# Optimization experiments

Measured on AMD Instinct MI355X. Metric: run time of the kernel, lower is better.

Reference implementation:

```python
import jax, jax.numpy as jnp
import numpy as np

PATCH = 14  # dinov2 patch size
LN_EPS = 1e-5


def setup_inputs() -> dict:
    key = jax.random.key(0)
    ks = jax.random.split(key, 6)
    Nb, P, E, Hd = 4096, 5476, 1024, 128  # boxes, patches (74*74), embed_dim, hidden_dim
    return {
        "patch_tokens": jax.random.normal(ks[0], (1, P, E), dtype=jnp.float32),
        "bboxes": jax.random.randint(ks[1], (Nb, 4), 0, 1036, dtype=jnp.int32),
        "H": 1036,
        "W": 1036,
        "W1": jax.random.normal(ks[2], (E, Hd), dtype=jnp.float32) * 0.02,
        "b1": jnp.zeros((Hd,), dtype=jnp.float32),
        "gamma": jnp.ones((Hd,), dtype=jnp.float32),
        "beta": jnp.zeros((Hd,), dtype=jnp.float32),
        "W2": jax.random.normal(ks[3], (Hd, Hd), dtype=jnp.float32) * 0.02,
        "b2": jnp.zeros((Hd,), dtype=jnp.float32),
    }


def _roi_pool(patch_tokens, bboxes, H, W):
    """Vectorized equivalent of VisionEncoder.roi_pool_patches.

    patch_tokens: (1, nph*npw, E); bboxes: (Nb, 4) int pixel coords.
    Returns (Nb, E) mean of patch tokens inside each box.
    """
    nph, npw = H // PATCH, W // PATCH
    Nb = bboxes.shape[0]
    x1, y1, x2, y2 = (bboxes[:, 0], bboxes[:, 1], bboxes[:, 2], bboxes[:, 3])
    f32 = jnp.float32
    # int() truncation in torch == astype(int32) for non-negative values
    px1 = (x1.astype(f32) / W * npw).astype(jnp.int32)
    px2 = (x2.astype(f32) / W * npw).astype(jnp.int32)
    py1 = (y1.astype(f32) / H * nph).astype(jnp.int32)
    py2 = (y2.astype(f32) / H * nph).astype(jnp.int32)
    px1 = jnp.clip(px1, 0, npw - 1)
    px2 = jnp.maximum(px1 + 1, jnp.minimum(px2, npw))
    py1 = jnp.clip(py1, 0, nph - 1)
    py2 = jnp.maximum(py1 + 1, jnp.minimum(py2, nph))
    # Box membership masks over the patch grid (ragged gather expressed densely)
    ay = jnp.arange(nph, dtype=jnp.int32)
    ax = jnp.arange(npw, dtype=jnp.int32)
    my = (ay[None, :] >= py1[:, None]) & (ay[None, :] < py2[:, None])  # (Nb, nph)
    mx = (ax[None, :] >= px1[:, None]) & (ax[None, :] < px2[:, None])  # (Nb, npw)
    mask = (my[:, :, None] & mx[:, None, :]).reshape(Nb, nph * npw)
    mask = mask.astype(patch_tokens.dtype)
    counts = mask.sum(axis=-1, keepdims=True)  # always >= 1 by construction
    pooled = (mask @ patch_tokens[0]) / counts  # (Nb, E)
    return pooled


def _projection(x, W1, b1, gamma, beta, W2, b2):
    h = x @ W1 + b1
    mu = h.mean(axis=-1, keepdims=True)
    var = ((h - mu) ** 2).mean(axis=-1, keepdims=True)
    h = (h - mu) * jax.lax.rsqrt(var + LN_EPS) * gamma + beta
    h = jax.nn.relu(h)
    return h @ W2 + b2


def reference(patch_tokens, bboxes, H, W, W1, b1, gamma, beta, W2, b2):
    pooled = _roi_pool(patch_tokens, bboxes, H, W)
    return _projection(pooled, W1, b1, gamma, beta, W2, b2)
```

## Files before the change

kernel.cpp:

```cpp
#include <hip/hip_runtime.h>


#define HD 128
#define SPLITK 8

__device__ __forceinline__ int decode_dim(const int* p, int fallback) {
    if (p == nullptr) return fallback;
    int vi = *p;
    if (vi >= 1 && vi <= 1000000) return vi;
    float vf = __int_as_float(vi);
    if (vf >= 1.0f && vf <= 1000000.0f) return (int)vf;
    return fallback;
}

__attribute__((noinline, optnone))
__device__ int coord_map(int x, int W, int n) {
    double rd = 1.0 / (double)W;
    float r = (float)rd;
    double qd = (double)x * (double)r;
    float q = (float)qd;
    double pd = (double)q * (double)n;
    float p = (float)pd;
    return (int)p;
}

__global__ __launch_bounds__(256) void gemm_u_kernel(
    const float* __restrict__ T, const float* __restrict__ W1,
    float* __restrict__ U, int P, int E)
{
    __shared__ float As[32][65];
    __shared__ float Bs[32][HD];

    int t  = threadIdx.x;
    int tc = t & 31;
    int tr = t >> 5;
    int row0 = blockIdx.x * 64;
    int ks   = blockIdx.y;
    int kchunk = E >> 3;
    int kbase  = ks * kchunk;
    float* Uo = U + (size_t)ks * (size_t)P * HD;

    float acc[8][4];
#pragma unroll
    for (int r = 0; r < 8; ++r)
#pragma unroll
        for (int j = 0; j < 4; ++j) acc[r][j] = 0.f;

    int arow = t >> 2;
    int akq  = (t & 3) * 8;
    int brow = t >> 5;
    int bc   = (t & 31) * 4;

    for (int kt = 0; kt < kchunk; kt += 32) {
        int k0 = kbase + kt;
        {
            int rg = row0 + arow; if (rg >= P) rg = P - 1;
            const float* tp = T + (size_t)rg * E + k0 + akq;
            float4 v0 = *(const float4*)tp;
            float4 v1 = *(const float4*)(tp + 4);
            As[akq + 0][arow] = v0.x; As[akq + 1][arow] = v0.y;
            As[akq + 2][arow] = v0.z; As[akq + 3][arow] = v0.w;
            As[akq + 4][arow] = v1.x; As[akq + 5][arow] = v1.y;
            As[akq + 6][arow] = v1.z; As[akq + 7][arow] = v1.w;
        }
#pragma unroll
        for (int i = 0; i < 4; ++i) {
            int kk = brow + i * 8;
            *(float4*)&Bs[kk][bc] =
                *(const float4*)&W1[(size_t)(k0 + kk) * HD + bc];
        }
        __syncthreads();

#pragma unroll
        for (int kk = 0; kk < 32; ++kk) {
            float4 a0 = *(const float4*)&As[kk][tr * 8];
            float4 a1 = *(const float4*)&As[kk][tr * 8 + 4];
            float4 b  = *(const float4*)&Bs[kk][tc * 4];
            float av[8] = {a0.x, a0.y, a0.z, a0.w, a1.x, a1.y, a1.z, a1.w};
            float bv[4] = {b.x, b.y, b.z, b.w};
#pragma unroll
            for (int r = 0; r < 8; ++r)
#pragma unroll
                for (int j = 0; j < 4; ++j)
                    acc[r][j] += av[r] * bv[j];
        }
        __syncthreads();
    }

#pragma unroll
    for (int r = 0; r < 8; ++r) {
        int p = row0 + tr * 8 + r;
        if (p < P) {
            float4 v = make_float4(acc[r][0], acc[r][1], acc[r][2], acc[r][3]);
            *(float4*)&Uo[(size_t)p * HD + tc * 4] = v;
        }
    }
}

__global__ __launch_bounds__(256) void prefix_x_kernel(
    const float* __restrict__ U, float* __restrict__ S,
    int P, int npw, int nph)
{
    extern __shared__ float tile[];
    int t = threadIdx.x;
    int y = blockIdx.x;
    int ch0 = blockIdx.y * 64;
    size_t ustride = (size_t)P * HD;
    size_t ubase = (size_t)y * npw * HD + ch0;

    int nj = npw * 16;
    for (int j = t; j < nj; j += 256) {
        int x = j >> 4, cq = (j & 15) * 4;
        size_t off = ubase + (size_t)x * HD + cq;
        float4 s = *(const float4*)(U + off);
#pragma unroll
        for (int p = 1; p < SPLITK; ++p) {
            float4 v = *(const float4*)(U + (size_t)p * ustride + off);
            s.x += v.x; s.y += v.y; s.z += v.z; s.w += v.w;
        }
        *(float4*)&tile[x * 64 + cq] = s;
    }
    __syncthreads();

    if (t < 64) {
        int c = t;
        size_t srow = (size_t)(y + 1) * (npw + 1) * HD + ch0;
        S[srow + c] = 0.f;
        float acc = 0.f;
        for (int x = 0; x < npw; ++x) {
            acc += tile[x * 64 + c];
            S[srow + (size_t)(x + 1) * HD + c] = acc;
        }
    }
}

__global__ __launch_bounds__(256) void prefix_y_kernel(
    float* __restrict__ S, int npw, int nph)
{
    extern __shared__ float tile[];
    int t = threadIdx.x;
    int x = blockIdx.x;
    int ch0 = blockIdx.y * 64;
    size_t stride = (size_t)(npw + 1) * HD;
    size_t base = (size_t)x * HD + ch0;

    int nj = nph * 16;
    for (int j = t; j < nj; j += 256) {
        int y = j >> 4, cq = (j & 15) * 4;
        *(float4*)&tile[y * 64 + cq] =
            *(const float4*)(S + base + (size_t)(y + 1) * stride + cq);
    }
    __syncthreads();

    if (t < 64) {
        int c = t;
        S[base + c] = 0.f;
        float acc = 0.f;
        for (int y = 0; y < nph; ++y) {
            acc += tile[y * 64 + c];
            S[base + (size_t)(y + 1) * stride + c] = acc;
        }
    }
}

__global__ __launch_bounds__(256) void pool_proj_kernel(
    const float* __restrict__ S, const int* __restrict__ bboxes,
    const int* __restrict__ pH, const int* __restrict__ pW,
    const float* __restrict__ b1, const float* __restrict__ gamma,
    const float* __restrict__ beta, const float* __restrict__ W2,
    const float* __restrict__ b2, float* __restrict__ out,
    int Nb, int npw, int nph, int fbW, int fbH)
{
    __shared__ float hs[16][HD + 1];
    __shared__ float Bs[32][HD];
    __shared__ float red_s[16][17], red_q[16][17];
    __shared__ int   cI11[16], cI12[16], cI21[16], cI22[16];
    __shared__ float cCnt[16];
    __shared__ float mu_s[16], rs_s[16];

    int t = threadIdx.x;
    int c = t & 127;
    int rh = t >> 7;
    int row0 = blockIdx.x * 16;

    if (t < 16) {
        int b = row0 + t; if (b >= Nb) b = Nb - 1;
        int x1 = bboxes[b * 4 + 0];
        int y1 = bboxes[b * 4 + 1];
        int x2 = bboxes[b * 4 + 2];
        int y2 = bboxes[b * 4 + 3];
        int Wi = decode_dim(pW, fbW);
        int Hi = decode_dim(pH, fbH);
        int px1 = coord_map(x1, Wi, npw);
        int px2 = coord_map(x2, Wi, npw);
        int py1 = coord_map(y1, Hi, nph);
        int py2 = coord_map(y2, Hi, nph);
        px1 = min(max(px1, 0), npw - 1);
        px2 = max(px1 + 1, min(px2, npw));
        py1 = min(max(py1, 0), nph - 1);
        py2 = max(py1 + 1, min(py2, nph));
        int st = npw + 1;
        cI11[t] = (py1 * st + px1) * HD;
        cI12[t] = (py1 * st + px2) * HD;
        cI21[t] = (py2 * st + px1) * HD;
        cI22[t] = (py2 * st + px2) * HD;
        cCnt[t] = (float)((py2 - py1) * (px2 - px1));
    }
    __syncthreads();

    float bias1 = b1[c];
    float hv[8];
#pragma unroll
    for (int r = 0; r < 8; ++r) {
        int row = rh * 8 + r;
        float s = S[cI22[row] + c] - S[cI12[row] + c]
                - S[cI21[row] + c] + S[cI11[row] + c];
        hv[r] = s / cCnt[row] + bias1;
        hs[row][c] = hv[r];
    }
    __syncthreads();

    {
        int sr = t & 15;
        int sg = t >> 4;
        float ps = 0.f, pq = 0.f;
#pragma unroll
        for (int i = 0; i < 8; ++i) {
            float v = hs[sr][sg * 8 + i];
            ps += v; pq += v * v;
        }
        red_s[sr][sg] = ps; red_q[sr][sg] = pq;
    }
    __syncthreads();
    if (t < 16) {
        float s = 0.f, q = 0.f;
#pragma unroll
        for (int i = 0; i < 16; ++i) { s += red_s[t][i]; q += red_q[t][i]; }
        float m = s * (1.0f / HD);
        float v = q * (1.0f / HD) - m * m;
        mu_s[t] = m;
        rs_s[t] = rsqrtf(v + 1e-5f);
    }
    __syncthreads();

    float g = gamma[c], be = beta[c];
#pragma unroll
    for (int r = 0; r < 8; ++r) {
        int row = rh * 8 + r;
        float x = (hv[r] - mu_s[row]) * rs_s[row] * g + be;
        hs[row][c] = fmaxf(x, 0.f);
    }
    __syncthreads();

    float bias2 = b2[c];
    float acc2[8];
#pragma unroll
    for (int r = 0; r < 8; ++r) acc2[r] = bias2;
    for (int k0 = 0; k0 < HD; k0 += 32) {
#pragma unroll
        for (int i = 0; i < 16; ++i) {
            int idx = t + i * 256;
            int kk = idx >> 7, cc = idx & 127;
            Bs[kk][cc] = W2[(size_t)(k0 + kk) * HD + cc];
        }
        __syncthreads();
#pragma unroll
        for (int kk = 0; kk < 32; ++kk) {
            float bv = Bs[kk][c];
#pragma unroll
            for (int r = 0; r < 8; ++r)
                acc2[r] += hs[rh * 8 + r][k0 + kk] * bv;
        }
        __syncthreads();
    }

#pragma unroll
    for (int r = 0; r < 8; ++r) {
        int rg = row0 + rh * 8 + r;
        if (rg < Nb) out[(size_t)rg * HD + c] = acc2[r];
    }
}

extern "C" void kernel_launch(void* const* d_in, const int* in_sizes, int n_in,
                              void* d_out, int out_size, void* d_ws, size_t ws_size,
                              hipStream_t stream) {
    int iT = 0, iB = 1, iH = 2, iW = 3, iW1 = 4, ib1 = 5, ig = 6, ibe = 7,
        iW2 = 8, ib2 = 9;
    bool has_scalars = (n_in >= 10 && in_sizes[2] == 1 && in_sizes[3] == 1);
    if (!has_scalars) { iW1 = 2; ib1 = 3; ig = 4; ibe = 5; iW2 = 6; ib2 = 7; }

    const float* tokens = (const float*)d_in[iT];
    const int*   bboxes = (const int*)d_in[iB];
    const int*   pH     = has_scalars ? (const int*)d_in[iH] : nullptr;
    const int*   pW     = has_scalars ? (const int*)d_in[iW] : nullptr;
    const float* W1     = (const float*)d_in[iW1];
    const float* b1     = (const float*)d_in[ib1];
    const float* gamma  = (const float*)d_in[ig];
    const float* beta   = (const float*)d_in[ibe];
    const float* W2     = (const float*)d_in[iW2];
    const float* b2     = (const float*)d_in[ib2];
    float* out = (float*)d_out;

    int Hd = in_sizes[ib1];
    int E  = in_sizes[iW1] / Hd;
    int Nb = in_sizes[iB] / 4;
    int P  = in_sizes[iT] / E;
    int npw = 1;
    while ((npw + 1) * (npw + 1) <= P) ++npw;
    int nph = P / npw;
    (void)out_size; (void)ws_size;

    float* S = (float*)d_ws;
    size_t s_elems = ((size_t)(nph + 1) * (npw + 1) * HD + 255) & ~(size_t)255;
    float* U = S + s_elems;

    int mtiles = (P + 63) / 64;
    gemm_u_kernel<<<dim3(mtiles, SPLITK), dim3(256), 0, stream>>>(
        tokens, W1, U, P, E);
    prefix_x_kernel<<<dim3(nph, 2), dim3(256), (size_t)npw * 64 * 4, stream>>>(
        U, S, P, npw, nph);
    prefix_y_kernel<<<dim3(npw + 1, 2), dim3(256), (size_t)nph * 64 * 4, stream>>>(
        S, npw, nph);
    pool_proj_kernel<<<dim3((Nb + 15) / 16), dim3(256), 0, stream>>>(
        S, bboxes, pH, pW, b1, gamma, beta, W2, b2, out, Nb, npw, nph,
        14 * npw, 14 * nph);
}
```

Baseline: 138.7 us.

## Compute token×W1 GEMM with split-bf16 MFMA instead of FP32 FMA

Replaces the FP32 shared-memory tiled GEMM (tokens × W1) with an MFMA kernel. It splits each FP32 value into bf16 hi and lo parts and accumulates three bf16 products per tile to keep close to FP32 accuracy. A new pre-kernel transposes W1 and splits it into hi/lo bf16 arrays, and split-K drops from 8 to 4, which halves the partial-sum writes read by the prefix stage. This adds an extra launch and workspace, drops shared-memory reuse of W1 in favour of direct global loads, and gives slightly different rounding than pure FP32.

```diff
diff --git a/kernel.cpp b/kernel.cpp
--- a/kernel.cpp
+++ b/kernel.cpp
@@ -2,7 +2,10 @@
 
 
 #define HD 128
-#define SPLITK 8
+#define SPLITK 4
+
+typedef __attribute__((ext_vector_type(8))) short bf16x8;
+typedef __attribute__((ext_vector_type(4))) float f32x4;
 
 __device__ __forceinline__ int decode_dim(const int* p, int fallback) {
     if (p == nullptr) return fallback;
@@ -24,75 +27,98 @@
     return (int)p;
 }
 
-__global__ __launch_bounds__(256) void gemm_u_kernel(
-    const float* __restrict__ T, const float* __restrict__ W1,
-    float* __restrict__ U, int P, int E)
-{
-    __shared__ float As[32][65];
-    __shared__ float Bs[32][HD];
-
-    int t  = threadIdx.x;
-    int tc = t & 31;
-    int tr = t >> 5;
-    int row0 = blockIdx.x * 64;
-    int ks   = blockIdx.y;
-    int kchunk = E >> 3;
-    int kbase  = ks * kchunk;
-    float* Uo = U + (size_t)ks * (size_t)P * HD;
-
-    float acc[8][4];
-#pragma unroll
-    for (int r = 0; r < 8; ++r)
-#pragma unroll
-        for (int j = 0; j < 4; ++j) acc[r][j] = 0.f;
-
-    int arow = t >> 2;
-    int akq  = (t & 3) * 8;
-    int brow = t >> 5;
-    int bc   = (t & 31) * 4;
+__global__ __launch_bounds__(256) void split_w1_kernel(
+    const float* __restrict__ W1, unsigned short* __restrict__ Whi,
+    unsigned short* __restrict__ Wlo, int E)
+{
+    __shared__ float tile[64][65];
+    int t = threadIdx.x;
+    int k0 = blockIdx.x * 64, n0 = blockIdx.y * 64;
+
+    int r = t >> 4, c4 = (t & 15) * 4;
+#pragma unroll
+    for (int i = 0; i < 4; ++i) {
+        int kr = r + i * 16;
+        *(float4*)&tile[kr][c4] =
+            *(const float4*)&W1[(size_t)(k0 + kr) * HD + n0 + c4];
+    }
+    __syncthreads();
+
+    int nl = t >> 2, kq = (t & 3) * 16;
+    unsigned hp[8], lp[8];
+#pragma unroll
+    for (int j = 0; j < 8; ++j) {
+        float x0 = tile[kq + 2 * j][nl];
+        float x1 = tile[kq + 2 * j + 1][nl];
+        unsigned u0 = __float_as_uint(x0);
+        unsigned u1 = __float_as_uint(x1);
+        float l0 = x0 - __uint_as_float(u0 & 0xffff0000u);
+        float l1 = x1 - __uint_as_float(u1 & 0xffff0000u);
+        hp[j] = (u0 >> 16) | (u1 & 0xffff0000u);
+        lp[j] = (__float_as_uint(l0) >> 16) | (__float_as_uint(l1) & 0xffff0000u);
+    }
+    size_t off = (size_t)(n0 + nl) * E + k0 + kq;
+    *(uint4*)(Whi + off)     = make_uint4(hp[0], hp[1], hp[2], hp[3]);
+    *(uint4*)(Whi + off + 8) = make_uint4(hp[4], hp[5], hp[6], hp[7]);
+    *(uint4*)(Wlo + off)     = make_uint4(lp[0], lp[1], lp[2], lp[3]);
+    *(uint4*)(Wlo + off + 8) = make_uint4(lp[4], lp[5], lp[6], lp[7]);
+}
+
+__global__ __launch_bounds__(256) void gemm_u_mfma(
+    const float* __restrict__ T, const unsigned short* __restrict__ Whi,
+    const unsigned short* __restrict__ Wlo, float* __restrict__ U,
+    int P, int E)
+{
+    int t = threadIdx.x;
+    int lane = t & 63;
+    int w = t >> 6;
+    int row0 = blockIdx.x * 64 + w * 16;
+    int kchunk = E >> 2;
+    int kbase = blockIdx.y * kchunk;
+    float* Uo = U + (size_t)blockIdx.y * (size_t)P * HD;
+
+    int lr  = lane & 15;
+    int lkq = (lane >> 4) * 8;
+
+    int arow = row0 + lr; if (arow >= P) arow = P - 1;
+    const float* ap = T + (size_t)arow * E + kbase + lkq;
+    const unsigned short* bh0 = Whi + (size_t)lr * E + kbase + lkq;
+    const unsigned short* bl0 = Wlo + (size_t)lr * E + kbase + lkq;
+
+    f32x4 acc[8];
+#pragma unroll
+    for (int n = 0; n < 8; ++n) acc[n] = (f32x4){0.f, 0.f, 0.f, 0.f};
 
     for (int kt = 0; kt < kchunk; kt += 32) {
-        int k0 = kbase + kt;
-        {
-            int rg = row0 + arow; if (rg >= P) rg = P - 1;
-            const float* tp = T + (size_t)rg * E + k0 + akq;
-            float4 v0 = *(const float4*)tp;
-            float4 v1 = *(const float4*)(tp + 4);
-            As[akq + 0][arow] = v0.x; As[akq + 1][arow] = v0.y;
-            As[akq + 2][arow] = v0.z; As[akq + 3][arow] = v0.w;
-            As[akq + 4][arow] = v1.x; As[akq + 5][arow] = v1.y;
-            As[akq + 6][arow] = v1.z; As[akq + 7][arow] = v1.w;
-        }
-#pragma unroll
-        for (int i = 0; i < 4; ++i) {
-            int kk = brow + i * 8;
-            *(float4*)&Bs[kk][bc] =
-                *(const float4*)&W1[(size_t)(k0 + kk) * HD + bc];
-        }
-        __syncthreads();
-
-#pragma unroll
-        for (int kk = 0; kk < 32; ++kk) {
-            float4 a0 = *(const float4*)&As[kk][tr * 8];
-            float4 a1 = *(const float4*)&As[kk][tr * 8 + 4];
-            float4 b  = *(const float4*)&Bs[kk][tc * 4];
-            float av[8] = {a0.x, a0.y, a0.z, a0.w, a1.x, a1.y, a1.z, a1.w};
-            float bv[4] = {b.x, b.y, b.z, b.w};
-#pragma unroll
-            for (int r = 0; r < 8; ++r)
-#pragma unroll
-                for (int j = 0; j < 4; ++j)
-                    acc[r][j] += av[r] * bv[j];
-        }
-        __syncthreads();
-    }
-
-#pragma unroll
-    for (int r = 0; r < 8; ++r) {
-        int p = row0 + tr * 8 + r;
-        if (p < P) {
-            float4 v = make_float4(acc[r][0], acc[r][1], acc[r][2], acc[r][3]);
-            *(float4*)&Uo[(size_t)p * HD + tc * 4] = v;
+        float4 a0 = *(const float4*)(ap + kt);
+        float4 a1 = *(const float4*)(ap + kt + 4);
+        float av[8] = {a0.x, a0.y, a0.z, a0.w, a1.x, a1.y, a1.z, a1.w};
+        bf16x8 ahi, alo;
+#pragma unroll
+        for (int j = 0; j < 8; ++j) {
+            unsigned u = __float_as_uint(av[j]);
+            ahi[j] = (short)(u >> 16);
+            float l = av[j] - __uint_as_float(u & 0xffff0000u);
+            alo[j] = (short)(__float_as_uint(l) >> 16);
+        }
+#pragma unroll
+        for (int n = 0; n < 8; ++n) {
+            bf16x8 bhi = *(const bf16x8*)(bh0 + (size_t)(n * 16) * E + kt);
+            bf16x8 blo = *(const bf16x8*)(bl0 + (size_t)(n * 16) * E + kt);
+            acc[n] = __builtin_amdgcn_mfma_f32_16x16x32_bf16(ahi, bhi, acc[n], 0, 0, 0);
+            acc[n] = __builtin_amdgcn_mfma_f32_16x16x32_bf16(alo, bhi, acc[n], 0, 0, 0);
+            acc[n] = __builtin_amdgcn_mfma_f32_16x16x32_bf16(ahi, blo, acc[n], 0, 0, 0);
+        }
+    }
+
+    int cr0 = row0 + (lane >> 4) * 4;
+    int cc  = lane & 15;
+#pragma unroll
+    for (int n = 0; n < 8; ++n) {
+#pragma unroll
+        for (int r = 0; r < 4; ++r) {
+            int p = cr0 + r;
+            if (p < P) Uo[(size_t)p * HD + n * 16 + cc] = acc[n][r];
         }
     }
 }
@@ -313,10 +339,16 @@
     float* S = (float*)d_ws;
     size_t s_elems = ((size_t)(nph + 1) * (npw + 1) * HD + 255) & ~(size_t)255;
     float* U = S + s_elems;
+    size_t u_elems = (size_t)SPLITK * (size_t)P * HD;
+    unsigned short* Whi = (unsigned short*)(U + u_elems);
+    unsigned short* Wlo = Whi + (size_t)E * HD;
+
+    split_w1_kernel<<<dim3(E / 64, HD / 64), dim3(256), 0, stream>>>(
+        W1, Whi, Wlo, E);
 
     int mtiles = (P + 63) / 64;
-    gemm_u_kernel<<<dim3(mtiles, SPLITK), dim3(256), 0, stream>>>(
-        tokens, W1, U, P, E);
+    gemm_u_mfma<<<dim3(mtiles, SPLITK), dim3(256), 0, stream>>>(
+        tokens, Whi, Wlo, U, P, E);
     prefix_x_kernel<<<dim3(nph, 2), dim3(256), (size_t)npw * 64 * 4, stream>>>(
         U, S, P, npw, nph);
     prefix_y_kernel<<<dim3(npw + 1, 2), dim3(256), (size_t)nph * 64 * 4, stream>>>(
```

Measured after the change: 149.4 us. 7.7% more time.
